# Kernel tuning notes

Hardware: AMD Instinct MI355X
Metric: run time of the kernel (lower is better)

Reference implementation:

```python
import jax, jax.numpy as jnp
import numpy as np

SUB_NO = 128
T_HIST = 100
T_DATA = 20000
SYN_B = 3
HIST_B = 3
FIX_VAR = 1.0


def _build_kern(delta, log_tau, K):
    # delta: (S,), log_tau: (B,), K: (S,B) -> kernel (S, T_HIST)
    t = jnp.maximum(jnp.arange(T_HIST, dtype=jnp.float32)[None, :] - delta[:, None], 0.0)  # (S,T)
    tt = t[:, :, None] / jnp.exp(log_tau)[None, None, :]  # (S,T,B)
    return jnp.einsum('stb,sb->st', tt * jnp.exp(-tt), K)


def setup_inputs() -> dict:
    key = jax.random.key(0)
    ks = jax.random.split(key, 5)
    S = SUB_NO
    return {
        'S_conv': jax.random.normal(ks[0], (T_DATA, S), jnp.float32),
        'Y_ancest': jax.random.normal(ks[1], (T_DATA, S), jnp.float32),
        'Z_ancest': jax.random.uniform(ks[2], (T_DATA, S), jnp.float32),
        'noise': jax.random.normal(ks[3], (T_DATA, S), jnp.float32),
        'C_den': jax.random.uniform(ks[4], (S, S), jnp.float32),
        'W_sub': jnp.ones(S, jnp.float32) * 0.25,
        'theta_syn': jnp.zeros(S, jnp.float32),
        'K_spike': jnp.ones((S, SYN_B), jnp.float32) * 0.01,
        'tau_spike': jnp.arange(1.6, 1.6 + SYN_B, dtype=jnp.float32),
        'delta_spike': jnp.zeros(S, jnp.float32),
        'theta_spike': jnp.ones(S, jnp.float32) * (-1.0),
        'W_spike': jnp.ones(S, jnp.float32) * 0.1,
        'tau_hist': jnp.arange(0.5, 0.5 + HIST_B * 0.5, 0.5, dtype=jnp.float32),
        'K_hist': jnp.zeros((S, HIST_B), jnp.float32),
        'delta_hist': jnp.zeros(S, jnp.float32),
    }


def _forward(S_conv, Y_ancest, Z_ancest, noise, C_den, W_sub, theta_syn,
             K_spike, tau_spike, delta_spike, theta_spike, W_spike,
             tau_hist, K_hist, delta_hist):
    S = SUB_NO
    # kernels, flipped as in torch (conv1d cross-correlation with flipped kernel)
    hist_kf = _build_kern(delta_hist, tau_hist, K_hist)[:, ::-1]      # (S,T_HIST)
    anc_kf = _build_kern(delta_spike, tau_spike, K_spike)[:, ::-1]    # (S,T_HIST)

    # Ancestor path has no recurrence -> hoist out of the time loop.
    # spike_ancest filtering: C_den is linear & time-independent, so project first,
    # then depthwise-convolve along time.
    Z_pad = jnp.concatenate([jnp.zeros((T_HIST, S), S_conv.dtype), Z_ancest], axis=0)  # (T+T_HIST,S)
    A = Z_pad @ C_den.T  # (T+T_HIST, S)
    conv = jax.lax.conv_general_dilated(
        A.T[None],                 # (1, S, T+T_HIST)
        anc_kf[:, None, :],        # (S, 1, T_HIST)
        window_strides=(1,), padding='VALID',
        dimension_numbers=('NCH', 'OIH', 'NCH'),
        feature_group_count=S)     # (1, S, T_DATA+1)
    filtered_ancest = conv[0].T[:T_DATA]  # (T_DATA, S)

    raw_ancest = Y_ancest @ C_den.T  # (T_DATA, S)
    base = S_conv + theta_syn + filtered_ancest + raw_ancest  # (T_DATA,S)
    sqrt_var = FIX_VAR ** 0.5

    def step(buf, inp):
        # buf: (S, T_HIST) rolling history of Z_out (most recent at index -1)
        b, n = inp
        fh = jnp.sum(buf * hist_kf, axis=1)            # grouped conv1d == per-channel dot
        x_out = jax.nn.sigmoid(b + fh)
        down = x_out * W_spike + theta_spike           # down_mu_Z_t == mu_Z_t (up_mu_Z=None)
        z_out = jax.nn.sigmoid(down + n * sqrt_var)
        buf = jnp.concatenate([buf[:, 1:], z_out[:, None]], axis=1)
        return buf, (x_out * W_sub, z_out, down)

    buf0 = jnp.zeros((S, T_HIST), S_conv.dtype)
    _, (final_Y, final_Z, mu_Z) = jax.lax.scan(step, buf0, (base, noise))
    return final_Y, final_Z, mu_Z, mu_Z


def reference(S_conv, Y_ancest, Z_ancest, noise, C_den, W_sub, theta_syn,
              K_spike, tau_spike, delta_spike, theta_spike, W_spike,
              tau_hist, K_hist, delta_hist):
    return _forward(S_conv, Y_ancest, Z_ancest, noise, C_den, W_sub, theta_syn,
                    K_spike, tau_spike, delta_spike, theta_spike, W_spike,
                    tau_hist, K_hist, delta_hist)
```

## Files before the change

### kernel.cpp

```cpp
#include <hip/hip_runtime.h>

#define T_DATA 20000
#define S_NO   128
#define T_HIST 100
#define NELEM  (T_DATA * S_NO)

__device__ __forceinline__ float sigm(float v) {
    return 1.0f / (1.0f + __expf(-v));
}

__global__ void __launch_bounds__(256) k1_prep(const float* __restrict__ C,
                        const float* __restrict__ K_spike,
                        const float* __restrict__ tau_spike,
                        const float* __restrict__ delta_spike,
                        const float* __restrict__ tau_hist,
                        const float* __restrict__ K_hist,
                        const float* __restrict__ delta_hist,
                        float* __restrict__ Ct,
                        float* __restrict__ anc_kT,
                        float* __restrict__ hist_k,
                        int* __restrict__ flag) {
    const int tid = threadIdx.x;
    const int b   = blockIdx.x;
    if (b < 16) {
#pragma unroll
        for (int i = 0; i < 4; ++i) {
            const int q = b * 1024 + i * 256 + tid;
            Ct[(q & 127) * S_NO + (q >> 7)] = C[q];
        }
        return;
    }
    const int s    = tid & 127;
    const int half = tid >> 7;
    {
        float d  = delta_spike[s];
        float i0 = __expf(-tau_spike[0]);
        float i1 = __expf(-tau_spike[1]);
        float i2 = __expf(-tau_spike[2]);
        float k0 = K_spike[s * 3 + 0], k1 = K_spike[s * 3 + 1], k2 = K_spike[s * 3 + 2];
        for (int j = half * 50; j < half * 50 + 50; ++j) {
            float t  = fmaxf((float)j - d, 0.0f);
            float x0 = t * i0, x1 = t * i1, x2 = t * i2;
            anc_kT[j * S_NO + s] =
                k0 * x0 * __expf(-x0) + k1 * x1 * __expf(-x1) + k2 * x2 * __expf(-x2);
        }
    }
    {
        float d  = delta_hist[s];
        float i0 = __expf(-tau_hist[0]);
        float i1 = __expf(-tau_hist[1]);
        float i2 = __expf(-tau_hist[2]);
        float k0 = K_hist[s * 3 + 0], k1 = K_hist[s * 3 + 1], k2 = K_hist[s * 3 + 2];
        for (int j = half * 50; j < half * 50 + 50; ++j) {
            float t  = fmaxf((float)j - d, 0.0f);
            float x0 = t * i0, x1 = t * i1, x2 = t * i2;
            hist_k[s * T_HIST + j] =
                k0 * x0 * __expf(-x0) + k1 * x1 * __expf(-x1) + k2 * x2 * __expf(-x2);
        }
    }
    if (tid == 0) *flag = 0;
    __syncthreads();
    if (tid < 128) {
        if (K_hist[s * 3] != 0.0f || K_hist[s * 3 + 1] != 0.0f || K_hist[s * 3 + 2] != 0.0f)
            atomicOr(flag, 1);
    }
}

__global__ void __launch_bounds__(256) k2_gemm(const float* __restrict__ Z,
                                               const float* __restrict__ Y,
                                               const float* __restrict__ Ct,
                                               float* __restrict__ A,
                                               float* __restrict__ R) {
    __shared__ float Zt[16][128];
    __shared__ float Yt[16][128];
    const int t0  = blockIdx.x * 16;
    const int tid = threadIdx.x;
    {
        const float4* Zg = (const float4*)(Z + t0 * S_NO);
        const float4* Yg = (const float4*)(Y + t0 * S_NO);
        float4* Zl = (float4*)&Zt[0][0];
        float4* Yl = (float4*)&Yt[0][0];
        for (int q = tid; q < 512; q += 256) { Zl[q] = Zg[q]; Yl[q] = Yg[q]; }
    }
    __syncthreads();
    const int s  = tid & 127;
    const int tb = (tid >> 7) * 8;
    float accA[8] = {0, 0, 0, 0, 0, 0, 0, 0};
    float accR[8] = {0, 0, 0, 0, 0, 0, 0, 0};
    for (int k4 = 0; k4 < 32; ++k4) {
        const float c0 = Ct[(k4 * 4 + 0) * S_NO + s];
        const float c1 = Ct[(k4 * 4 + 1) * S_NO + s];
        const float c2 = Ct[(k4 * 4 + 2) * S_NO + s];
        const float c3 = Ct[(k4 * 4 + 3) * S_NO + s];
#pragma unroll
        for (int i = 0; i < 8; ++i) {
            float4 z = *(const float4*)&Zt[tb + i][k4 * 4];
            accA[i] = fmaf(c0, z.x, fmaf(c1, z.y, fmaf(c2, z.z, fmaf(c3, z.w, accA[i]))));
            float4 y = *(const float4*)&Yt[tb + i][k4 * 4];
            accR[i] = fmaf(c0, y.x, fmaf(c1, y.y, fmaf(c2, y.z, fmaf(c3, y.w, accR[i]))));
        }
    }
#pragma unroll
    for (int i = 0; i < 8; ++i) {
        A[(t0 + tb + i) * S_NO + s] = accA[i];
        R[(t0 + tb + i) * S_NO + s] = accR[i];
    }
}

__global__ void __launch_bounds__(256) k3_fused(const float* __restrict__ A,
                                                const float* __restrict__ anc_kT,
                                                const float* __restrict__ S_conv,
                                                const float* __restrict__ noise,
                                                const float* __restrict__ W_sub,
                                                const float* __restrict__ theta_syn,
                                                const float* __restrict__ theta_spike,
                                                const float* __restrict__ W_spike,
                                                const int* __restrict__ flag,
                                                float* __restrict__ out0,
                                                float* __restrict__ out1,
                                                float* __restrict__ out2,
                                                float* __restrict__ out3,
                                                float* __restrict__ Fws) {
    __shared__ float Al[141 * 64];
    const int tstart = blockIdx.x * 40;
    const int shalf  = blockIdx.y;
    const int tid    = threadIdx.x;
    for (int q = tid; q < 140 * 16; q += 256) {
        const int row = q >> 4, c4 = q & 15;
        const int u  = tstart - 100 + row;
        float4 v = make_float4(0.f, 0.f, 0.f, 0.f);
        if (u >= 0) v = *(const float4*)&A[u * S_NO + shalf * 64 + c4 * 4];
        *(float4*)&Al[(row + 1) * 64 + c4 * 4] = v;
    }
    __syncthreads();
    const int sl    = tid & 63;
    const int tg    = tid >> 6;
    const int sg    = shalf * 64 + sl;
    const int rbase = tg * 10;
    float acc[10] = {0, 0, 0, 0, 0, 0, 0, 0, 0, 0};
    float W[10];
#pragma unroll
    for (int i = 0; i < 10; ++i) W[i] = Al[(rbase + 100 + i) * 64 + sl];
#pragma unroll 10
    for (int j = 0; j < 100; ++j) {
        const float kv = anc_kT[j * S_NO + sg];
#pragma unroll
        for (int i = 0; i < 10; ++i)
            acc[i] = fmaf(W[(((i - j) % 10) + 10) % 10], kv, acc[i]);
        W[(10 - ((j + 1) % 10)) % 10] = Al[(rbase + 99 - j) * 64 + sl];
    }
    const int T0 = tstart + rbase;
    if (*flag == 0) {
        const float tsy = theta_syn[sg], wsub = W_sub[sg];
        const float wsp = W_spike[sg],  tsp  = theta_spike[sg];
#pragma unroll
        for (int i = 0; i < 10; ++i) {
            const int n = (T0 + i) * S_NO + sg;
            const float basev = S_conv[n] + tsy + out1[n] + acc[i];
            const float x  = sigm(basev);
            const float dn = fmaf(x, wsp, tsp);
            const float z  = sigm(dn + noise[n]);
            out0[n] = x * wsub;
            out1[n] = z;
            out2[n] = dn;
            out3[n] = dn;
        }
    } else {
#pragma unroll
        for (int i = 0; i < 10; ++i) Fws[(T0 + i) * S_NO + sg] = acc[i];
    }
}

__global__ void __launch_bounds__(64) k4_scan(const float* __restrict__ S_conv,
                                              const float* __restrict__ noise,
                                              const float* __restrict__ W_sub,
                                              const float* __restrict__ theta_syn,
                                              const float* __restrict__ theta_spike,
                                              const float* __restrict__ W_spike,
                                              const float* __restrict__ hist_k,
                                              const int* __restrict__ flag,
                                              const float* __restrict__ Fws,
                                              float* __restrict__ out0,
                                              float* __restrict__ out1,
                                              float* __restrict__ out2,
                                              float* __restrict__ out3) {
    if (*flag == 0) return;
    __shared__ float zr[128];
    const int s = blockIdx.x;
    const int l = threadIdx.x;
    zr[l] = 0.0f; zr[l + 64] = 0.0f;
    const float hk0 = (l < T_HIST) ? hist_k[s * T_HIST + l] : 0.0f;
    const float hk1 = (l + 64 < T_HIST) ? hist_k[s * T_HIST + l + 64] : 0.0f;
    const float tsy = theta_syn[s], wsub = W_sub[s];
    const float wsp = W_spike[s],  tsp  = theta_spike[s];
    for (int t = 0; t < T_DATA; ++t) {
        float fh = hk0 * zr[(t - 1 - l) & 127];
        fh = fmaf(hk1, zr[(t - 65 - l) & 127], fh);
#pragma unroll
        for (int m = 1; m < 64; m <<= 1) fh += __shfl_xor(fh, m, 64);
        const int n = t * S_NO + s;
        const float basev = S_conv[n] + tsy + out1[n] + Fws[n];
        const float x  = sigm(basev + fh);
        const float dn = fmaf(x, wsp, tsp);
        const float z  = sigm(dn + noise[n]);
        if (l == 0) {
            out0[n] = x * wsub;
            out1[n] = z;
            out2[n] = dn;
            out3[n] = dn;
            zr[t & 127] = z;
        }
    }
}

extern "C" void kernel_launch(void* const* d_in, const int* in_sizes, int n_in,
                              void* d_out, int out_size, void* d_ws, size_t ws_size,
                              hipStream_t stream) {
    const float* S_conv  = (const float*)d_in[0];
    const float* Y_anc   = (const float*)d_in[1];
    const float* Z_anc   = (const float*)d_in[2];
    const float* noise   = (const float*)d_in[3];
    const float* C_den   = (const float*)d_in[4];
    const float* W_sub   = (const float*)d_in[5];
    const float* th_syn  = (const float*)d_in[6];
    const float* K_spk   = (const float*)d_in[7];
    const float* tau_spk = (const float*)d_in[8];
    const float* dl_spk  = (const float*)d_in[9];
    const float* th_spk  = (const float*)d_in[10];
    const float* W_spk   = (const float*)d_in[11];
    const float* tau_h   = (const float*)d_in[12];
    const float* K_h     = (const float*)d_in[13];
    const float* dl_h    = (const float*)d_in[14];

    float* out  = (float*)d_out;
    float* out0 = out;
    float* out1 = out + NELEM;
    float* out2 = out + 2 * NELEM;
    float* out3 = out + 3 * NELEM;

    float* ws     = (float*)d_ws;
    float* wsA    = ws;
    float* wsF    = ws + NELEM;
    float* Ct     = ws + 2 * NELEM;
    float* anc_kT = Ct + 16384;
    float* hist_k = anc_kT + T_HIST * S_NO;
    int*   flag   = (int*)(hist_k + S_NO * T_HIST);

    k1_prep<<<17, 256, 0, stream>>>(C_den, K_spk, tau_spk, dl_spk, tau_h, K_h, dl_h,
                                    Ct, anc_kT, hist_k, flag);
    k2_gemm<<<T_DATA / 16, 256, 0, stream>>>(Z_anc, Y_anc, Ct, wsA, out1);
    k3_fused<<<dim3(T_DATA / 40, 2), 256, 0, stream>>>(wsA, anc_kT, S_conv, noise,
                                                       W_sub, th_syn, th_spk, W_spk,
                                                       flag, out0, out1, out2, out3, wsF);
    k4_scan<<<S_NO, 64, 0, stream>>>(S_conv, noise, W_sub, th_syn, th_spk, W_spk,
                                     hist_k, flag, wsF, out0, out1, out2, out3);
}
```

Before: 189.7 us.

## Register-tile ancestor GEMM with float4 outputs and restructure time conv without LDS

The projection GEMM now processes 32 time rows per block, and each thread computes a 4x4 tile with float4 loads of the transposed C matrix and float4 stores. The depthwise ancestor convolution drops its shared-memory staging. Each thread instead computes 16 consecutive outputs by loading 31-sample windows straight from global memory, in 16-tap chunks over a kernel zero-padded to 112 taps. The aim is more register reuse and fewer LDS round trips. The cost is higher register pressure, some redundant global/L2 reads of A, and a few extra padded taps.

Result: faster. 169.0 us (-10.9%).

```diff
diff --git a/kernel.cpp b/kernel.cpp
--- a/kernel.cpp
+++ b/kernel.cpp
@@ -3,10 +3,16 @@
 #define T_DATA 20000
 #define S_NO   128
 #define T_HIST 100
+#define J_PAD  112
 #define NELEM  (T_DATA * S_NO)
 
 __device__ __forceinline__ float sigm(float v) {
     return 1.0f / (1.0f + __expf(-v));
+}
+
+__device__ __forceinline__ void fma4(float4& a, float s, const float4 c) {
+    a.x = fmaf(s, c.x, a.x); a.y = fmaf(s, c.y, a.y);
+    a.z = fmaf(s, c.z, a.z); a.w = fmaf(s, c.w, a.w);
 }
 
 __global__ void __launch_bounds__(256) k1_prep(const float* __restrict__ C,
@@ -38,11 +44,14 @@
         float i1 = __expf(-tau_spike[1]);
         float i2 = __expf(-tau_spike[2]);
         float k0 = K_spike[s * 3 + 0], k1 = K_spike[s * 3 + 1], k2 = K_spike[s * 3 + 2];
-        for (int j = half * 50; j < half * 50 + 50; ++j) {
-            float t  = fmaxf((float)j - d, 0.0f);
-            float x0 = t * i0, x1 = t * i1, x2 = t * i2;
-            anc_kT[j * S_NO + s] =
-                k0 * x0 * __expf(-x0) + k1 * x1 * __expf(-x1) + k2 * x2 * __expf(-x2);
+        for (int j = half * 56; j < half * 56 + 56; ++j) {
+            float v = 0.0f;
+            if (j < T_HIST) {
+                float t  = fmaxf((float)j - d, 0.0f);
+                float x0 = t * i0, x1 = t * i1, x2 = t * i2;
+                v = k0 * x0 * __expf(-x0) + k1 * x1 * __expf(-x1) + k2 * x2 * __expf(-x2);
+            }
+            anc_kT[j * S_NO + s] = v;
         }
     }
     {
@@ -71,39 +80,68 @@
                                                const float* __restrict__ Ct,
                                                float* __restrict__ A,
                                                float* __restrict__ R) {
-    __shared__ float Zt[16][128];
-    __shared__ float Yt[16][128];
-    const int t0  = blockIdx.x * 16;
+    __shared__ float Zt[32 * 128];
+    __shared__ float Yt[32 * 128];
+    const int t0  = blockIdx.x * 32;
     const int tid = threadIdx.x;
     {
         const float4* Zg = (const float4*)(Z + t0 * S_NO);
         const float4* Yg = (const float4*)(Y + t0 * S_NO);
-        float4* Zl = (float4*)&Zt[0][0];
-        float4* Yl = (float4*)&Yt[0][0];
-        for (int q = tid; q < 512; q += 256) { Zl[q] = Zg[q]; Yl[q] = Yg[q]; }
+        float4* Zl = (float4*)Zt;
+        float4* Yl = (float4*)Yt;
+        for (int q = tid; q < 1024; q += 256) { Zl[q] = Zg[q]; Yl[q] = Yg[q]; }
     }
     __syncthreads();
-    const int s  = tid & 127;
-    const int tb = (tid >> 7) * 8;
-    float accA[8] = {0, 0, 0, 0, 0, 0, 0, 0};
-    float accR[8] = {0, 0, 0, 0, 0, 0, 0, 0};
+    const int sg = tid & 31;
+    const int tg = tid >> 5;
+    const int s0 = sg * 4;
+    float4 accA[4] = {{0,0,0,0},{0,0,0,0},{0,0,0,0},{0,0,0,0}};
+    float4 accR[4] = {{0,0,0,0},{0,0,0,0},{0,0,0,0},{0,0,0,0}};
     for (int k4 = 0; k4 < 32; ++k4) {
-        const float c0 = Ct[(k4 * 4 + 0) * S_NO + s];
-        const float c1 = Ct[(k4 * 4 + 1) * S_NO + s];
-        const float c2 = Ct[(k4 * 4 + 2) * S_NO + s];
-        const float c3 = Ct[(k4 * 4 + 3) * S_NO + s];
-#pragma unroll
-        for (int i = 0; i < 8; ++i) {
-            float4 z = *(const float4*)&Zt[tb + i][k4 * 4];
-            accA[i] = fmaf(c0, z.x, fmaf(c1, z.y, fmaf(c2, z.z, fmaf(c3, z.w, accA[i]))));
-            float4 y = *(const float4*)&Yt[tb + i][k4 * 4];
-            accR[i] = fmaf(c0, y.x, fmaf(c1, y.y, fmaf(c2, y.z, fmaf(c3, y.w, accR[i]))));
-        }
-    }
-#pragma unroll
-    for (int i = 0; i < 8; ++i) {
-        A[(t0 + tb + i) * S_NO + s] = accA[i];
-        R[(t0 + tb + i) * S_NO + s] = accR[i];
+        const float4 c0 = *(const float4*)&Ct[(k4 * 4 + 0) * S_NO + s0];
+        const float4 c1 = *(const float4*)&Ct[(k4 * 4 + 1) * S_NO + s0];
+        const float4 c2 = *(const float4*)&Ct[(k4 * 4 + 2) * S_NO + s0];
+        const float4 c3 = *(const float4*)&Ct[(k4 * 4 + 3) * S_NO + s0];
+#pragma unroll
+        for (int i = 0; i < 4; ++i) {
+            const float4 z = *(const float4*)&Zt[(tg * 4 + i) * S_NO + k4 * 4];
+            fma4(accA[i], z.x, c0); fma4(accA[i], z.y, c1);
+            fma4(accA[i], z.z, c2); fma4(accA[i], z.w, c3);
+            const float4 y = *(const float4*)&Yt[(tg * 4 + i) * S_NO + k4 * 4];
+            fma4(accR[i], y.x, c0); fma4(accR[i], y.y, c1);
+            fma4(accR[i], y.z, c2); fma4(accR[i], y.w, c3);
+        }
+    }
+#pragma unroll
+    for (int i = 0; i < 4; ++i) {
+        *(float4*)&A[(t0 + tg * 4 + i) * S_NO + s0] = accA[i];
+        *(float4*)&R[(t0 + tg * 4 + i) * S_NO + s0] = accR[i];
+    }
+}
+
+template <bool GUARD>
+__device__ __forceinline__ void conv16(const float* __restrict__ A,
+                                       const float* __restrict__ kT,
+                                       int t0, int s, float acc[16]) {
+    for (int c = 0; c < 7; ++c) {
+        const int B = t0 - 16 * c - 16;
+        float w[31];
+        float kj[16];
+#pragma unroll
+        for (int q = 0; q < 31; ++q) {
+            const int u = B + q;
+            if (GUARD)
+                w[q] = (u >= 0) ? A[u * S_NO + s] : 0.0f;
+            else
+                w[q] = A[u * S_NO + s];
+        }
+#pragma unroll
+        for (int r = 0; r < 16; ++r) kj[r] = kT[(16 * c + r) * S_NO + s];
+#pragma unroll
+        for (int r = 0; r < 16; ++r)
+#pragma unroll
+            for (int i = 0; i < 16; ++i)
+                acc[i] = fmaf(kj[r], w[i + 15 - r], acc[i]);
     }
 }
 
@@ -121,43 +159,21 @@
                                                 float* __restrict__ out2,
                                                 float* __restrict__ out3,
                                                 float* __restrict__ Fws) {
-    __shared__ float Al[141 * 64];
-    const int tstart = blockIdx.x * 40;
-    const int shalf  = blockIdx.y;
-    const int tid    = threadIdx.x;
-    for (int q = tid; q < 140 * 16; q += 256) {
-        const int row = q >> 4, c4 = q & 15;
-        const int u  = tstart - 100 + row;
-        float4 v = make_float4(0.f, 0.f, 0.f, 0.f);
-        if (u >= 0) v = *(const float4*)&A[u * S_NO + shalf * 64 + c4 * 4];
-        *(float4*)&Al[(row + 1) * 64 + c4 * 4] = v;
-    }
-    __syncthreads();
-    const int sl    = tid & 63;
-    const int tg    = tid >> 6;
-    const int sg    = shalf * 64 + sl;
-    const int rbase = tg * 10;
-    float acc[10] = {0, 0, 0, 0, 0, 0, 0, 0, 0, 0};
-    float W[10];
-#pragma unroll
-    for (int i = 0; i < 10; ++i) W[i] = Al[(rbase + 100 + i) * 64 + sl];
-#pragma unroll 10
-    for (int j = 0; j < 100; ++j) {
-        const float kv = anc_kT[j * S_NO + sg];
-#pragma unroll
-        for (int i = 0; i < 10; ++i)
-            acc[i] = fmaf(W[(((i - j) % 10) + 10) % 10], kv, acc[i]);
-        W[(10 - ((j + 1) % 10)) % 10] = Al[(rbase + 99 - j) * 64 + sl];
-    }
-    const int T0 = tstart + rbase;
+    const int tid = threadIdx.x;
+    const int s   = tid & 127;
+    const int tg  = tid >> 7;
+    const int t0  = blockIdx.x * 32 + tg * 16;
+    float acc[16] = {0,0,0,0,0,0,0,0,0,0,0,0,0,0,0,0};
+    if (t0 >= J_PAD) conv16<false>(A, anc_kT, t0, s, acc);
+    else             conv16<true >(A, anc_kT, t0, s, acc);
+
     if (*flag == 0) {
-        const float tsy = theta_syn[sg], wsub = W_sub[sg];
-        const float wsp = W_spike[sg],  tsp  = theta_spike[sg];
-#pragma unroll
-        for (int i = 0; i < 10; ++i) {
-            const int n = (T0 + i) * S_NO + sg;
-            const float basev = S_conv[n] + tsy + out1[n] + acc[i];
-            const float x  = sigm(basev);
+        const float tsy = theta_syn[s], wsub = W_sub[s];
+        const float wsp = W_spike[s],  tsp  = theta_spike[s];
+#pragma unroll
+        for (int i = 0; i < 16; ++i) {
+            const int n = (t0 + i) * S_NO + s;
+            const float x  = sigm(S_conv[n] + tsy + out1[n] + acc[i]);
             const float dn = fmaf(x, wsp, tsp);
             const float z  = sigm(dn + noise[n]);
             out0[n] = x * wsub;
@@ -167,7 +183,7 @@
         }
     } else {
 #pragma unroll
-        for (int i = 0; i < 10; ++i) Fws[(T0 + i) * S_NO + sg] = acc[i];
+        for (int i = 0; i < 16; ++i) Fws[(t0 + i) * S_NO + s] = acc[i];
     }
 }
 
@@ -242,16 +258,16 @@
     float* wsA    = ws;
     float* wsF    = ws + NELEM;
     float* Ct     = ws + 2 * NELEM;
-    float* anc_kT = Ct + 16384;
-    float* hist_k = anc_kT + T_HIST * S_NO;
+    float* anc_kT = Ct + S_NO * S_NO;
+    float* hist_k = anc_kT + J_PAD * S_NO;
     int*   flag   = (int*)(hist_k + S_NO * T_HIST);
 
     k1_prep<<<17, 256, 0, stream>>>(C_den, K_spk, tau_spk, dl_spk, tau_h, K_h, dl_h,
                                     Ct, anc_kT, hist_k, flag);
-    k2_gemm<<<T_DATA / 16, 256, 0, stream>>>(Z_anc, Y_anc, Ct, wsA, out1);
-    k3_fused<<<dim3(T_DATA / 40, 2), 256, 0, stream>>>(wsA, anc_kT, S_conv, noise,
-                                                       W_sub, th_syn, th_spk, W_spk,
-                                                       flag, out0, out1, out2, out3, wsF);
+    k2_gemm<<<T_DATA / 32, 256, 0, stream>>>(Z_anc, Y_anc, Ct, wsA, out1);
+    k3_fused<<<T_DATA / 32, 256, 0, stream>>>(wsA, anc_kT, S_conv, noise,
+                                              W_sub, th_syn, th_spk, W_spk,
+                                              flag, out0, out1, out2, out3, wsF);
     k4_scan<<<S_NO, 64, 0, stream>>>(S_conv, noise, W_sub, th_syn, th_spk, W_spk,
                                      hist_k, flag, wsF, out0, out1, out2, out3);
 }
```
